# Kernel optimization log

Measured on AMD Instinct MI355X. Metric: run time of the kernel, lower is better.

The kernel has to match this reference:

```python
import jax, jax.numpy as jnp
import numpy as np

N, D = 16384, 128
T = 0.07  # temperature


def setup_inputs() -> dict:
    key = jax.random.key(0)
    x = jax.random.normal(key, (N, D), dtype=jnp.float32)
    # uniformity loss assumes unit-norm embeddings (else exp(||x||^2 / t) overflows)
    x = x / jnp.linalg.norm(x, axis=-1, keepdims=True)
    return {"x": x}


def reference(x):
    # x.matmul(x.T).div(t).exp().sum(-1).log().mean()
    sims = jnp.matmul(x, x.T) / T            # [N, N]
    return jnp.mean(jnp.log(jnp.sum(jnp.exp(sims), axis=-1)))
```

## Files before the change

kernel.cpp:

```cpp
#include <hip/hip_runtime.h>
#include <hip/hip_bf16.h>

#define NN 16384
#define DD 128
#define BM 128
#define BCOLS 4096
#define TCOLS 64
#define TILES 64
#define NBLOCKS 512
#define SQRT_SCALE 4.5398159622f

#define EXP_A 8388608.0f
#define EXP_K 1064986316.0f

typedef __attribute__((ext_vector_type(8))) short bf16x8;
typedef __attribute__((ext_vector_type(4))) float f32x4;

__global__ void convert_swz(const float* __restrict__ x, ushort* __restrict__ xb) {
    int t = blockIdx.x * blockDim.x + threadIdx.x;
    int r = t >> 4;
    int c = t & 15;
    const float4* src = (const float4*)(x + (size_t)r * DD + c * 8);
    float4 f0 = src[0];
    float4 f1 = src[1];
    float vals[8] = {f0.x, f0.y, f0.z, f0.w, f1.x, f1.y, f1.z, f1.w};
    bf16x8 v;
#pragma unroll
    for (int i = 0; i < 8; ++i) {
        __hip_bfloat16 h = __float2bfloat16(vals[i] * SQRT_SCALE);
        v[i] = (short)__builtin_bit_cast(unsigned short, h);
    }
    int cs = c ^ (r & 15);
    *(bf16x8*)(xb + (size_t)r * DD + cs * 8) = v;
}

__global__ __launch_bounds__(512, 4) void gemm_exp_stream(const ushort* __restrict__ xb,
                                                          float* __restrict__ rowsumP) {
    __shared__ __align__(16) char lds[8][2][4096];

    const int tid  = threadIdx.x;
    const int lane = tid & 63;
    const int wid  = tid >> 6;
    const int frow = lane & 15;
    const int kq   = lane >> 4;

    const int bid    = blockIdx.x;
    const int cq     = (bid & 7) >> 1;
    const int rstrip = ((bid >> 3) << 1) | (bid & 1);
    const int rw = wid >> 2;
    const int cw = wid & 3;
    const int R0 = rstrip * BM;
    const int C0 = cq * BCOLS;

    char* myL = &lds[wid][0][0];

    auto stage = [&](int buf, int t) {
        const char* g = (const char*)(xb + (size_t)(C0 + t * TCOLS + cw * 16) * DD);
#pragma unroll
        for (int j = 0; j < 4; ++j) {
            __builtin_amdgcn_global_load_lds(
                (const __attribute__((address_space(1))) unsigned int*)(g + j * 1024 + lane * 16),
                (__attribute__((address_space(3))) unsigned int*)(myL + buf * 4096 + j * 1024),
                16, 0, 0);
        }
    };

    stage(0, 0);
    stage(1, 1);

    bf16x8 af[4][4];
#pragma unroll
    for (int m = 0; m < 4; ++m)
#pragma unroll
        for (int kk = 0; kk < 4; ++kk) {
            int ra = R0 + rw * 64 + m * 16 + frow;
            int slot = (kk * 4 + kq) ^ frow;
            af[m][kk] = *(const bf16x8*)(xb + (size_t)ra * DD + slot * 8);
        }

    int roff[4];
#pragma unroll
    for (int kk = 0; kk < 4; ++kk)
        roff[kk] = frow * 256 + ((((kk << 2) + kq) ^ frow) << 4);

    asm volatile("s_waitcnt vmcnt(0)" ::: "memory");

    const f32x4 zacc = {0.f, 0.f, 0.f, 0.f};
    float rs[4][4] = {};

    for (int t = 0; t < TILES; ++t) {
        const int cur = t & 1;
        const char* Bb = myL + cur * 4096;

        f32x4 acc[4];
        __builtin_amdgcn_s_setprio(1);
#pragma unroll
        for (int kk = 0; kk < 4; ++kk) {
            bf16x8 bfr = *(const bf16x8*)(Bb + roff[kk]);
            if (kk == 0) {
#pragma unroll
                for (int m = 0; m < 4; ++m)
                    acc[m] = __builtin_amdgcn_mfma_f32_16x16x32_bf16(
                        af[m][0], bfr, zacc, 0, 0, 0);
            } else {
#pragma unroll
                for (int m = 0; m < 4; ++m)
                    acc[m] = __builtin_amdgcn_mfma_f32_16x16x32_bf16(
                        af[m][kk], bfr, acc[m], 0, 0, 0);
            }
        }
        __builtin_amdgcn_s_setprio(0);

        __builtin_amdgcn_sched_barrier(0);
        if (t + 2 < TILES) stage(cur, t + 2);

#pragma unroll
        for (int m = 0; m < 4; ++m)
#pragma unroll
            for (int j = 0; j < 4; ++j) {
                float b = __builtin_fmaf(acc[m][j], EXP_A, EXP_K);
                rs[m][j] += __builtin_bit_cast(float, (int)b);
            }

        if (t < TILES - 2)
            asm volatile("s_waitcnt vmcnt(4)" ::: "memory");
        else if (t == TILES - 2)
            asm volatile("s_waitcnt vmcnt(0)" ::: "memory");
    }

#pragma unroll
    for (int m = 0; m < 4; ++m)
#pragma unroll
        for (int j = 0; j < 4; ++j) {
            float s = rs[m][j];
            s += __shfl_xor(s, 1);
            s += __shfl_xor(s, 2);
            s += __shfl_xor(s, 4);
            s += __shfl_xor(s, 8);
            rs[m][j] = s;
        }

    if (frow == 0) {
        const int p = cq * 4 + cw;
        float* dst = rowsumP + (size_t)p * NN + R0 + rw * 64 + kq * 4;
#pragma unroll
        for (int m = 0; m < 4; ++m) {
            float4 v = {rs[m][0], rs[m][1], rs[m][2], rs[m][3]};
            *(float4*)(dst + m * 16) = v;
        }
    }
}

__global__ void finalize_part(const float* __restrict__ rowsumP,
                              float* __restrict__ partial) {
    const int tid = threadIdx.x;
    const int r = blockIdx.x * 256 + tid;
    float rsum = 0.f;
#pragma unroll
    for (int p = 0; p < 16; ++p)
        rsum += rowsumP[p * NN + r];
    float s = __builtin_amdgcn_logf(rsum) * 0.69314718056f;
#pragma unroll
    for (int o = 1; o < 64; o <<= 1)
        s += __shfl_xor(s, o);
    __shared__ float wsum[4];
    if ((tid & 63) == 0) wsum[tid >> 6] = s;
    __syncthreads();
    if (tid == 0)
        partial[blockIdx.x] = wsum[0] + wsum[1] + wsum[2] + wsum[3];
}

__global__ void finalize_sum(const float* __restrict__ partial, float* __restrict__ out) {
    float s = partial[threadIdx.x];
#pragma unroll
    for (int o = 1; o < 64; o <<= 1)
        s += __shfl_xor(s, o);
    if (threadIdx.x == 0)
        out[0] = s * (1.0f / NN);
}

extern "C" void kernel_launch(void* const* d_in, const int* in_sizes, int n_in,
                              void* d_out, int out_size, void* d_ws, size_t ws_size,
                              hipStream_t stream) {
    const float* x = (const float*)d_in[0];
    float* out = (float*)d_out;

    ushort* xb     = (ushort*)d_ws;
    float* rowsumP = (float*)((char*)d_ws + (size_t)NN * DD * 2);
    float* partial = rowsumP + 16 * NN;

    convert_swz<<<(NN * 16) / 256, 256, 0, stream>>>(x, xb);
    gemm_exp_stream<<<NBLOCKS, 512, 0, stream>>>(xb, rowsumP);
    finalize_part<<<64, 256, 0, stream>>>(rowsumP, partial);
    finalize_sum<<<1, 64, 0, stream>>>(partial, out);
}
```

Baseline: 86.39 us.

## Exploit symmetry of x·xᵀ by computing only upper-triangular tiles

Because x·xᵀ is symmetric, the GEMM now covers only the upper-triangular 64x64 tiles, about half the full matrix. Each tile's exp values are added to the row sums for its row strip and, through column sums, to the mirrored rows. Tiles are split evenly across 1024 blocks by walking a linear triangular index, and results go to a single rowsum buffer with atomicAdd instead of 16 partial buffers. The cost is extra shuffle reductions, frequent atomics, A-fragment reloads with full waits at strip boundaries, a memset, and order-dependent float summation.

```diff
diff --git a/kernel.cpp b/kernel.cpp
--- a/kernel.cpp
+++ b/kernel.cpp
@@ -3,11 +3,10 @@
 
 #define NN 16384
 #define DD 128
-#define BM 128
-#define BCOLS 4096
-#define TCOLS 64
-#define TILES 64
-#define NBLOCKS 512
+#define TS 64
+#define NS 256
+#define NTILES 32896
+#define NB 1024
 #define SQRT_SCALE 4.5398159622f
 
 #define EXP_A 8388608.0f
@@ -15,6 +14,8 @@
 
 typedef __attribute__((ext_vector_type(8))) short bf16x8;
 typedef __attribute__((ext_vector_type(4))) float f32x4;
+
+#define TRI(s) (256 * (s) - ((s) * ((s)-1)) / 2)
 
 __global__ void convert_swz(const float* __restrict__ x, ushort* __restrict__ xb) {
     int t = blockIdx.x * blockDim.x + threadIdx.x;
@@ -34,28 +35,32 @@
     *(bf16x8*)(xb + (size_t)r * DD + cs * 8) = v;
 }
 
-__global__ __launch_bounds__(512, 4) void gemm_exp_stream(const ushort* __restrict__ xb,
-                                                          float* __restrict__ rowsumP) {
-    __shared__ __align__(16) char lds[8][2][4096];
+__global__ __launch_bounds__(256, 4) void gemm_exp_tri(const ushort* __restrict__ xb,
+                                                       float* __restrict__ rowsum) {
+    __shared__ __align__(16) char lds[4][2][4096];
 
     const int tid  = threadIdx.x;
     const int lane = tid & 63;
-    const int wid  = tid >> 6;
+    const int cw   = tid >> 6;
     const int frow = lane & 15;
     const int kq   = lane >> 4;
 
-    const int bid    = blockIdx.x;
-    const int cq     = (bid & 7) >> 1;
-    const int rstrip = ((bid >> 3) << 1) | (bid & 1);
-    const int rw = wid >> 2;
-    const int cw = wid & 3;
-    const int R0 = rstrip * BM;
-    const int C0 = cq * BCOLS;
-
-    char* myL = &lds[wid][0][0];
-
-    auto stage = [&](int buf, int t) {
-        const char* g = (const char*)(xb + (size_t)(C0 + t * TCOLS + cw * 16) * DD);
+    char* myL = &lds[cw][0][0];
+
+    const int bid = blockIdx.x;
+    const int R0 = (int)(((long long)bid * NTILES) >> 10);
+    const int R1 = (int)(((long long)(bid + 1) * NTILES) >> 10);
+    const int n  = R1 - R0;
+
+    int s = (int)(256.5f - sqrtf(256.5f * 256.5f - 2.0f * (float)R0));
+    if (s < 0) s = 0;
+    if (s > 255) s = 255;
+    while (s < 255 && TRI(s + 1) <= R0) ++s;
+    while (s > 0 && TRI(s) > R0) --s;
+    int ct = s + (R0 - TRI(s));
+
+    auto stage = [&](int buf, int c) {
+        const char* g = (const char*)(xb + (size_t)(c * TS + cw * 16) * DD);
 #pragma unroll
         for (int j = 0; j < 4; ++j) {
             __builtin_amdgcn_global_load_lds(
@@ -65,18 +70,24 @@
         }
     };
 
-    stage(0, 0);
-    stage(1, 1);
+    int ps = s, pc = ct;
+    stage(0, pc);
+    if (pc == 255) { ++ps; pc = ps; } else ++pc;
+    stage(1, pc);
+    if (pc == 255) { ++ps; pc = ps; } else ++pc;
 
     bf16x8 af[4][4];
-#pragma unroll
-    for (int m = 0; m < 4; ++m)
-#pragma unroll
-        for (int kk = 0; kk < 4; ++kk) {
-            int ra = R0 + rw * 64 + m * 16 + frow;
-            int slot = (kk * 4 + kq) ^ frow;
-            af[m][kk] = *(const bf16x8*)(xb + (size_t)ra * DD + slot * 8);
-        }
+    auto load_af = [&](int ss) {
+#pragma unroll
+        for (int m = 0; m < 4; ++m)
+#pragma unroll
+            for (int kk = 0; kk < 4; ++kk) {
+                int ra = ss * TS + m * 16 + frow;
+                int slot = (kk * 4 + kq) ^ frow;
+                af[m][kk] = *(const bf16x8*)(xb + (size_t)ra * DD + slot * 8);
+            }
+    };
+    load_af(s);
 
     int roff[4];
 #pragma unroll
@@ -88,8 +99,29 @@
     const f32x4 zacc = {0.f, 0.f, 0.f, 0.f};
     float rs[4][4] = {};
 
-    for (int t = 0; t < TILES; ++t) {
-        const int cur = t & 1;
+    auto flush_rows = [&](int ss) {
+#pragma unroll
+        for (int m = 0; m < 4; ++m)
+#pragma unroll
+            for (int j = 0; j < 4; ++j) {
+                float v = rs[m][j];
+                v += __shfl_xor(v, 1);
+                v += __shfl_xor(v, 2);
+                v += __shfl_xor(v, 4);
+                v += __shfl_xor(v, 8);
+                rs[m][j] = v;
+            }
+        if (frow == 0) {
+#pragma unroll
+            for (int m = 0; m < 4; ++m)
+#pragma unroll
+                for (int j = 0; j < 4; ++j)
+                    atomicAdd(&rowsum[ss * TS + m * 16 + kq * 4 + j], rs[m][j]);
+        }
+    };
+
+    for (int q = 0; q < n; ++q) {
+        const int cur = q & 1;
         const char* Bb = myL + cur * 4096;
 
         f32x4 acc[4];
@@ -112,54 +144,54 @@
         __builtin_amdgcn_s_setprio(0);
 
         __builtin_amdgcn_sched_barrier(0);
-        if (t + 2 < TILES) stage(cur, t + 2);
-
+        if (q + 2 < n) {
+            stage(cur, pc);
+            if (pc == 255) { ++ps; pc = ps; } else ++pc;
+        }
+
+        float cs = 0.f;
 #pragma unroll
         for (int m = 0; m < 4; ++m)
 #pragma unroll
             for (int j = 0; j < 4; ++j) {
                 float b = __builtin_fmaf(acc[m][j], EXP_A, EXP_K);
-                rs[m][j] += __builtin_bit_cast(float, (int)b);
-            }
-
-        if (t < TILES - 2)
-            asm volatile("s_waitcnt vmcnt(4)" ::: "memory");
-        else if (t == TILES - 2)
-            asm volatile("s_waitcnt vmcnt(0)" ::: "memory");
+                float e = __builtin_bit_cast(float, (int)b);
+                rs[m][j] += e;
+                cs += e;
+            }
+        cs += __shfl_xor(cs, 16);
+        cs += __shfl_xor(cs, 32);
+        if (ct != s && kq == 0)
+            atomicAdd(&rowsum[ct * TS + cw * 16 + frow], cs);
+
+        if (q + 1 < n) {
+            int olds = s;
+            if (ct == 255) { ++s; ct = s; } else ++ct;
+            if (s != olds) {
+                flush_rows(olds);
+#pragma unroll
+                for (int m = 0; m < 4; ++m)
+#pragma unroll
+                    for (int j = 0; j < 4; ++j)
+                        rs[m][j] = 0.f;
+                load_af(s);
+                asm volatile("s_waitcnt vmcnt(0)" ::: "memory");
+            } else if (q < n - 2) {
+                asm volatile("s_waitcnt vmcnt(4)" ::: "memory");
+            } else {
+                asm volatile("s_waitcnt vmcnt(0)" ::: "memory");
+            }
+        }
     }
 
-#pragma unroll
-    for (int m = 0; m < 4; ++m)
-#pragma unroll
-        for (int j = 0; j < 4; ++j) {
-            float s = rs[m][j];
-            s += __shfl_xor(s, 1);
-            s += __shfl_xor(s, 2);
-            s += __shfl_xor(s, 4);
-            s += __shfl_xor(s, 8);
-            rs[m][j] = s;
-        }
-
-    if (frow == 0) {
-        const int p = cq * 4 + cw;
-        float* dst = rowsumP + (size_t)p * NN + R0 + rw * 64 + kq * 4;
-#pragma unroll
-        for (int m = 0; m < 4; ++m) {
-            float4 v = {rs[m][0], rs[m][1], rs[m][2], rs[m][3]};
-            *(float4*)(dst + m * 16) = v;
-        }
-    }
-}
-
-__global__ void finalize_part(const float* __restrict__ rowsumP,
+    flush_rows(s);
+}
+
+__global__ void finalize_part(const float* __restrict__ rowsum,
                               float* __restrict__ partial) {
     const int tid = threadIdx.x;
     const int r = blockIdx.x * 256 + tid;
-    float rsum = 0.f;
-#pragma unroll
-    for (int p = 0; p < 16; ++p)
-        rsum += rowsumP[p * NN + r];
-    float s = __builtin_amdgcn_logf(rsum) * 0.69314718056f;
+    float s = __builtin_amdgcn_logf(rowsum[r]) * 0.69314718056f;
 #pragma unroll
     for (int o = 1; o < 64; o <<= 1)
         s += __shfl_xor(s, o);
@@ -186,11 +218,12 @@
     float* out = (float*)d_out;
 
     ushort* xb     = (ushort*)d_ws;
-    float* rowsumP = (float*)((char*)d_ws + (size_t)NN * DD * 2);
-    float* partial = rowsumP + 16 * NN;
-
+    float* rowsum  = (float*)((char*)d_ws + (size_t)NN * DD * 2);
+    float* partial = rowsum + NN;
+
+    hipMemsetAsync(rowsum, 0, NN * sizeof(float), stream);
     convert_swz<<<(NN * 16) / 256, 256, 0, stream>>>(x, xb);
-    gemm_exp_stream<<<NBLOCKS, 512, 0, stream>>>(xb, rowsumP);
-    finalize_part<<<64, 256, 0, stream>>>(rowsumP, partial);
+    gemm_exp_tri<<<NB, 256, 0, stream>>>(xb, rowsum);
+    finalize_part<<<64, 256, 0, stream>>>(rowsum, partial);
     finalize_sum<<<1, 64, 0, stream>>>(partial, out);
 }
```

New measurement: 86.77 us. Within noise of the previous version (+0.4%).
